# Kernel tuning notes

Measured on AMD Instinct MI355X. Metric: run time of the kernel, lower is better.

## Reference

```python
import jax, jax.numpy as jnp
import numpy as np
import math

H = 8
D_MODEL = 512
D_K = D_MODEL // H          # 64, per-head value dim
D_QK = D_K // 2             # 32, per-head query/key dim
B, S = 2, 4096


def setup_inputs() -> dict:
    key = jax.random.key(0)
    ks = jax.random.split(key, 20)
    std = 0.02
    inp = {
        'query': jax.random.normal(ks[0], (B, S, D_MODEL), jnp.float32),
        'key':   jax.random.normal(ks[1], (B, S, D_MODEL), jnp.float32),
        'value': jax.random.normal(ks[2], (B, S, D_MODEL), jnp.float32),
        # MLP_q: d_model -> 2*d_model -> d_model/2
        'Wq1': jax.random.normal(ks[3], (D_MODEL, 2 * D_MODEL), jnp.float32) * std,
        'bq1': jnp.zeros((2 * D_MODEL,), jnp.float32),
        'Wq2': jax.random.normal(ks[4], (2 * D_MODEL, D_MODEL // 2), jnp.float32) * std,
        'bq2': jnp.zeros((D_MODEL // 2,), jnp.float32),
        # MLP_k: d_model -> 2*d_model -> d_model/2
        'Wk1': jax.random.normal(ks[5], (D_MODEL, 2 * D_MODEL), jnp.float32) * std,
        'bk1': jnp.zeros((2 * D_MODEL,), jnp.float32),
        'Wk2': jax.random.normal(ks[6], (2 * D_MODEL, D_MODEL // 2), jnp.float32) * std,
        'bk2': jnp.zeros((D_MODEL // 2,), jnp.float32),
        # linear_v and output linear: d_model -> d_model
        'Wv': jax.random.normal(ks[7], (D_MODEL, D_MODEL), jnp.float32) * std,
        'bv': jnp.zeros((D_MODEL,), jnp.float32),
        'Wo': jax.random.normal(ks[8], (D_MODEL, D_MODEL), jnp.float32) * std,
        'bo': jnp.zeros((D_MODEL,), jnp.float32),
    }
    return inp


def reference(query, key, value, Wq1, bq1, Wq2, bq2, Wk1, bk1, Wk2, bk2, Wv, bv, Wo, bo):
    nb = query.shape[0]
    # MLP_q / MLP_k: Linear -> exact GELU -> Linear (torch GELU default is erf)
    q = jax.nn.gelu(query @ Wq1 + bq1, approximate=False) @ Wq2 + bq2   # [B,S,D_MODEL/2]
    k = jax.nn.gelu(key   @ Wk1 + bk1, approximate=False) @ Wk2 + bk2   # [B,S,D_MODEL/2]
    v = value @ Wv + bv                                                  # [B,S,D_MODEL]

    q = q.reshape(nb, -1, H, D_QK)   # [B,S,H,d_qk]
    k = k.reshape(nb, -1, H, D_QK)
    v = v.reshape(nb, -1, H, D_K)    # [B,S,H,d_k]

    # scores scaled by sqrt(d_qk) since query.size(-1) == d_k//2 in the original
    scores = jnp.einsum('bqhd,bkhd->bhqk', q, k) / math.sqrt(D_QK)  # [B,H,S,S]
    p = jax.nn.softmax(scores, axis=-1)
    x = jnp.einsum('bhqk,bkhd->bqhd', p, v).reshape(nb, -1, H * D_K)  # [B,S,D_MODEL]
    return x @ Wo + bo
```

## Files before the change

### kernel.cpp

```cpp
#include <hip/hip_runtime.h>
#include <math.h>

typedef __attribute__((ext_vector_type(8))) short short8;
typedef __bf16 bf16x8 __attribute__((ext_vector_type(8)));
typedef __attribute__((ext_vector_type(4))) float f32x4;
typedef __attribute__((ext_vector_type(2))) float f32x2;
typedef __attribute__((ext_vector_type(16))) float f32x16;
typedef __attribute__((ext_vector_type(4))) unsigned uint4v;

__device__ inline short f2bf(float f) {
    unsigned u = __builtin_bit_cast(unsigned, f);
    u += 0x7fff + ((u >> 16) & 1);
    return (short)(u >> 16);
}
__device__ inline float gelu_f(float x) {
    return 0.5f * x * (1.f + erff(x * 0.70710678118654752f));
}

__device__ inline void gload_lds16(const void* g, void* l) {
    __builtin_amdgcn_global_load_lds(
        (const __attribute__((address_space(1))) unsigned int*)g,
        (__attribute__((address_space(3))) unsigned int*)l, 16, 0, 0);
}

__global__ __launch_bounds__(256) void prep_w(
    const float* __restrict__ Wq1, const float* __restrict__ Wk1,
    const float* __restrict__ Wq2, const float* __restrict__ Wk2,
    const float* __restrict__ Wv,  const float* __restrict__ Wo,
    short* __restrict__ Wq1t, short* __restrict__ Wk1t,
    short* __restrict__ Wq2t, short* __restrict__ Wk2t,
    short* __restrict__ Wvt,  short* __restrict__ Wot)
{
    int id = blockIdx.x;
    const float* W; short* Wt; int K, N;
    if (id < 512)       { W = Wq1; Wt = Wq1t; K = 512;  N = 1024; }
    else if (id < 1024) { W = Wk1; Wt = Wk1t; K = 512;  N = 1024; id -= 512; }
    else if (id < 1280) { W = Wq2; Wt = Wq2t; K = 1024; N = 256;  id -= 1024; }
    else if (id < 1536) { W = Wk2; Wt = Wk2t; K = 1024; N = 256;  id -= 1280; }
    else if (id < 1792) { W = Wv;  Wt = Wvt;  K = 512;  N = 512;  id -= 1536; }
    else                { W = Wo;  Wt = Wot;  K = 512;  N = 512;  id -= 1792; }
    int nx = N >> 5;
    int n0 = (id % nx) * 32, k0 = (id / nx) * 32;

    __shared__ float T[32][33];
    int tid = threadIdx.x;
    int r = tid >> 3, c4 = (tid & 7) * 4;
    float4 v4 = *(const float4*)&W[(size_t)(k0 + r) * N + n0 + c4];
    T[r][c4 + 0] = v4.x; T[r][c4 + 1] = v4.y; T[r][c4 + 2] = v4.z; T[r][c4 + 3] = v4.w;
    __syncthreads();
    short4 o;
    o.x = f2bf(T[c4 + 0][r]);
    o.y = f2bf(T[c4 + 1][r]);
    o.z = f2bf(T[c4 + 2][r]);
    o.w = f2bf(T[c4 + 3][r]);
    *(short4*)&Wt[(size_t)(n0 + r) * K + k0 + c4] = o;
}

template <int BM, int BN, int AF32>
__device__ __forceinline__ void gemm_core(
    const void* __restrict__ A, const short* __restrict__ B,
    const float* __restrict__ bias, void* __restrict__ C_,
    float scale, int act, int om, int nbn, int N, int K, int L)
{
    constexpr int MT = BM / 32;
    constexpr int NT = BN / 32;
    const int xcd = L & 7;
    const int per = L >> 3;
    const int bn = (per % nbn) * BN;
    const int bm = ((per / nbn) * 8 + xcd) * BM;

    const int tid = threadIdx.x;
    const int w = tid >> 6;
    const int lane = tid & 63;
    const int l15 = lane & 15, quad = lane >> 4;
    const int wm = (w >> 1) * (BM / 2), wn = (w & 1) * (BN / 2);

    __shared__ __align__(16) short As0[BM * 64], As1[BM * 64];
    __shared__ __align__(16) short Bs0[BN * 64], Bs1[BN * 64];

    const float* Af = (const float*)A;
    const short* Ab = (const short*)A;

    float4 xa[BM / 32], ya[BM / 32];

    auto issue = [&](int k0, short* Asb, short* Bsb) {
#pragma unroll
        for (int i = 0; i < BM / 32; ++i) {
            int ga = tid + i * 256;
            int row = ga >> 3, g = ga & 7;
            if constexpr (AF32) {
                const float* src = &Af[(size_t)(bm + row) * K + k0 + ((g ^ (row & 7)) * 8)];
                xa[i] = *(const float4*)src;
                ya[i] = *(const float4*)(src + 4);
            } else {
                gload_lds16(&Ab[(size_t)(bm + row) * K + k0 + ((g ^ (row & 7)) * 8)],
                            &Asb[(i * 256 + w * 64) * 8]);
            }
        }
#pragma unroll
        for (int i = 0; i < BN / 32; ++i) {
            int gb = tid + i * 256;
            int row = gb >> 3, g = gb & 7;
            gload_lds16(&B[(size_t)(bn + row) * K + k0 + ((g ^ (row & 7)) * 8)],
                        &Bsb[(i * 256 + w * 64) * 8]);
        }
    };
    auto finishA = [&](short* Asb) {
        if constexpr (AF32) {
#pragma unroll
            for (int i = 0; i < BM / 32; ++i) {
                int ga = tid + i * 256;
                int row = ga >> 3, g = ga & 7;
                unsigned u0, u1, u2, u3;
                asm("v_cvt_pk_bf16_f32 %0, %1, %2" : "=v"(u0) : "v"(xa[i].x), "v"(xa[i].y));
                asm("v_cvt_pk_bf16_f32 %0, %1, %2" : "=v"(u1) : "v"(xa[i].z), "v"(xa[i].w));
                asm("v_cvt_pk_bf16_f32 %0, %1, %2" : "=v"(u2) : "v"(ya[i].x), "v"(ya[i].y));
                asm("v_cvt_pk_bf16_f32 %0, %1, %2" : "=v"(u3) : "v"(ya[i].z), "v"(ya[i].w));
                uint4v u; u[0] = u0; u[1] = u1; u[2] = u2; u[3] = u3;
                *(uint4v*)(void*)&Asb[row * 64 + g * 8] = u;
            }
        }
    };

    f32x4 acc[MT][NT];
#pragma unroll
    for (int mt = 0; mt < MT; ++mt)
#pragma unroll
        for (int nt = 0; nt < NT; ++nt) acc[mt][nt] = (f32x4){0.f, 0.f, 0.f, 0.f};

    auto compute = [&](const short* Asc, const short* Bsc) {
#pragma unroll
        for (int ks = 0; ks < 2; ++ks) {
            bf16x8 af[MT], bfr[NT];
#pragma unroll
            for (int t2 = 0; t2 < MT; ++t2) {
                int row = wm + t2 * 16 + l15;
                af[t2] = __builtin_bit_cast(bf16x8,
                    *(const short8*)(const void*)&Asc[row * 64 + (((ks * 4 + quad) ^ (row & 7)) * 8)]);
            }
#pragma unroll
            for (int t2 = 0; t2 < NT; ++t2) {
                int row = wn + t2 * 16 + l15;
                bfr[t2] = __builtin_bit_cast(bf16x8,
                    *(const short8*)(const void*)&Bsc[row * 64 + (((ks * 4 + quad) ^ (row & 7)) * 8)]);
            }
#pragma unroll
            for (int mt = 0; mt < MT; ++mt)
#pragma unroll
                for (int nt = 0; nt < NT; ++nt)
                    acc[mt][nt] = __builtin_amdgcn_mfma_f32_16x16x32_bf16(af[mt], bfr[nt], acc[mt][nt], 0, 0, 0);
        }
    };

    const int ntile = K >> 6;

    issue(0, As0, Bs0);
    finishA(As0);
    __syncthreads();

    for (int t = 0; t < ntile; t += 2) {
        issue((t + 1) << 6, As1, Bs1);
        compute(As0, Bs0);
        finishA(As1);
        __syncthreads();
        if (t + 2 < ntile) issue((t + 2) << 6, As0, Bs0);
        compute(As1, Bs1);
        if (t + 2 < ntile) finishA(As0);
        __syncthreads();
    }

    float bvv[NT];
#pragma unroll
    for (int nt = 0; nt < NT; ++nt) bvv[nt] = bias[bn + wn + nt * 16 + l15];
#pragma unroll
    for (int mt = 0; mt < MT; ++mt)
#pragma unroll
        for (int r = 0; r < 4; ++r) {
            int row = bm + wm + mt * 16 + quad * 4 + r;
#pragma unroll
            for (int nt = 0; nt < NT; ++nt) {
                float v = acc[mt][nt][r] + bvv[nt];
                if (act) v = gelu_f(v);
                v *= scale;
                int col = bn + wn + nt * 16 + l15;
                if (om == 1) {
                    ((float*)C_)[(size_t)row * N + col] = v;
                } else if (om == 2) {
                    int b_ = row >> 12, key = row & 4095;
                    int kt = key >> 6, nt_ = (key >> 5) & 1, l31_ = key & 31;
                    int h_ = col >> 5, kcol = col & 31;
                    int ks_ = kcol >> 4, hi_ = (kcol >> 3) & 1, j_ = kcol & 7;
                    size_t idx = ((((size_t)(b_ * 8 + h_) * 64 + kt) * 4 +
                                   (nt_ * 2 + ks_)) * 64 + (hi_ * 32 + l31_)) * 8 + j_;
                    ((short*)C_)[idx] = f2bf(v);
                } else if (om == 3) {
                    int b_ = row >> 12, key = row & 4095;
                    int kt = key >> 6, keyr = key & 63;
                    int ks_ = keyr >> 4, hi_ = (keyr >> 3) & 1, j_ = keyr & 7;
                    int h_ = col >> 6, dk = col & 63;
                    int dt_ = dk >> 5, l31_ = dk & 31;
                    size_t idx = ((((size_t)(b_ * 8 + h_) * 64 + kt) * 8 +
                                   (dt_ * 4 + ks_)) * 64 + (hi_ * 32 + l31_)) * 8 + j_;
                    ((short*)C_)[idx] = f2bf(v);
                } else {
                    ((short*)C_)[(size_t)row * N + col] = f2bf(v);
                }
            }
        }
}

__global__ __launch_bounds__(256) void mega1(
    const float* __restrict__ q, const float* __restrict__ k,
    const float* __restrict__ v,
    const short* __restrict__ Wq1t, const short* __restrict__ Wk1t,
    const short* __restrict__ Wvt,
    const float* __restrict__ bq1, const float* __restrict__ bk1,
    const float* __restrict__ bv,
    short* __restrict__ H1q, short* __restrict__ H1k, short* __restrict__ vfr)
{
    const int z = blockIdx.z;
    if (z == 2 && blockIdx.x >= 1024) return;
    const float* A   = z == 2 ? v    : (z == 1 ? k    : q);
    const short* B   = z == 2 ? Wvt  : (z == 1 ? Wk1t : Wq1t);
    const float* bia = z == 2 ? bv   : (z == 1 ? bk1  : bq1);
    void*        C   = z == 2 ? (void*)vfr : (z == 1 ? (void*)H1k : (void*)H1q);
    const int act = z == 2 ? 0 : 1;
    const int om  = z == 2 ? 3 : 0;
    const int nbn = z == 2 ? 8 : 16;
    const int N   = z == 2 ? 512 : 1024;
    gemm_core<64, 64, 1>(A, B, bia, C, 1.f, act, om, nbn, N, 512, blockIdx.x);
}

__global__ __launch_bounds__(256) void gemm2k(
    const short* __restrict__ H1q, const short* __restrict__ H1k,
    const short* __restrict__ Wq2t, const short* __restrict__ Wk2t,
    const float* __restrict__ bq2, const float* __restrict__ bk2,
    short* __restrict__ qbb, short* __restrict__ kfr, float qscale)
{
    const int z = blockIdx.z;
    const short* A   = z ? H1k : H1q;
    const short* B   = z ? Wk2t : Wq2t;
    const float* bia = z ? bk2 : bq2;
    void*        C   = z ? (void*)kfr : (void*)qbb;
    const float  sc  = z ? 1.f : qscale;
    const int    om  = z ? 2 : 0;
    gemm_core<64, 64, 0>(A, B, bia, C, sc, 0, om, 4, 256, 1024, blockIdx.x);
}

__global__ __launch_bounds__(256) void gemmok(
    const short* __restrict__ xbb, const short* __restrict__ Wot,
    const float* __restrict__ bo, float* __restrict__ out)
{
    gemm_core<64, 64, 0>(xbb, Wot, bo, out, 1.f, 0, 1, 8, 512, 512, blockIdx.x);
}

__global__ __launch_bounds__(256, 4) void flash_ks(
    const short* __restrict__ qb, const short* __restrict__ kfr,
    const short* __restrict__ vfr, short* __restrict__ xbb)
{
    const int L = blockIdx.x;
    const int xcd = L & 7;
    const int idx = L >> 3;
    const int bh = xcd * 2 + (idx & 1);
    const int qt = idx >> 1;
    const int b = bh >> 3, h = bh & 7;
    const int w = threadIdx.x >> 6;
    const int qg = w >> 1;
    const int kh = w & 1;
    const int lane = threadIdx.x & 63;
    const int l31 = lane & 31;
    const int half = lane >> 5;

    __shared__ __align__(16) char smem[17408];

    const short* qrow = qb + (size_t)(b * 4096 + qt * 64 + qg * 32 + l31) * 256 + h * 32 + half * 8;
    bf16x8 qf0 = __builtin_bit_cast(bf16x8, *(const short8*)(const void*)qrow);
    bf16x8 qf1 = __builtin_bit_cast(bf16x8, *(const short8*)(const void*)(qrow + 16));

    f32x16 O0{}, O1{};
    f32x2 lp = (f32x2){0.f, 0.f};

    const short* kbase = kfr + ((size_t)bh * 64) * 4 * 512 + lane * 8;
    const short* vbase = vfr + ((size_t)bh * 64) * 8 * 512 + lane * 8;

#pragma unroll 1
    for (int t = 0; t < 32; ++t) {
        const int kt = kh * 32 + t;
        bf16x8 kc[4], vc[8];
        const short* kp = kbase + (size_t)kt * 4 * 512;
        const short* vp = vbase + (size_t)kt * 8 * 512;
#pragma unroll
        for (int c = 0; c < 4; ++c)
            kc[c] = __builtin_bit_cast(bf16x8, *(const short8*)(const void*)(kp + c * 512));
#pragma unroll
        for (int c = 0; c < 8; ++c)
            vc[c] = __builtin_bit_cast(bf16x8, *(const short8*)(const void*)(vp + c * 512));

        f32x16 zero{};
        f32x16 s0 = __builtin_amdgcn_mfma_f32_32x32x16_bf16(kc[0], qf0, zero, 0, 0, 0);
        s0 = __builtin_amdgcn_mfma_f32_32x32x16_bf16(kc[1], qf1, s0, 0, 0, 0);
        f32x16 s1 = __builtin_amdgcn_mfma_f32_32x32x16_bf16(kc[2], qf0, zero, 0, 0, 0);
        s1 = __builtin_amdgcn_mfma_f32_32x32x16_bf16(kc[3], qf1, s1, 0, 0, 0);

        bf16x8 pf[4];
#pragma unroll
        for (int nt = 0; nt < 2; ++nt) {
            const f32x16& s = nt ? s1 : s0;
            float p0  = __builtin_amdgcn_exp2f(s[0]);
            float p1  = __builtin_amdgcn_exp2f(s[1]);
            float p2  = __builtin_amdgcn_exp2f(s[2]);
            float p3  = __builtin_amdgcn_exp2f(s[3]);
            float p4  = __builtin_amdgcn_exp2f(s[4]);
            float p5  = __builtin_amdgcn_exp2f(s[5]);
            float p6  = __builtin_amdgcn_exp2f(s[6]);
            float p7  = __builtin_amdgcn_exp2f(s[7]);
            float p8  = __builtin_amdgcn_exp2f(s[8]);
            float p9  = __builtin_amdgcn_exp2f(s[9]);
            float p10 = __builtin_amdgcn_exp2f(s[10]);
            float p11 = __builtin_amdgcn_exp2f(s[11]);
            float p12 = __builtin_amdgcn_exp2f(s[12]);
            float p13 = __builtin_amdgcn_exp2f(s[13]);
            float p14 = __builtin_amdgcn_exp2f(s[14]);
            float p15 = __builtin_amdgcn_exp2f(s[15]);

            lp += (f32x2){p0,  p1};
            lp += (f32x2){p2,  p3};
            lp += (f32x2){p4,  p5};
            lp += (f32x2){p6,  p7};
            lp += (f32x2){p8,  p9};
            lp += (f32x2){p10, p11};
            lp += (f32x2){p12, p13};
            lp += (f32x2){p14, p15};

            unsigned D0, D1, D2, D3, D4, D5, D6, D7;
            asm("v_cvt_pk_bf16_f32 %0, %1, %2" : "=v"(D0) : "v"(p0),  "v"(p1));
            asm("v_cvt_pk_bf16_f32 %0, %1, %2" : "=v"(D1) : "v"(p2),  "v"(p3));
            asm("v_cvt_pk_bf16_f32 %0, %1, %2" : "=v"(D2) : "v"(p4),  "v"(p5));
            asm("v_cvt_pk_bf16_f32 %0, %1, %2" : "=v"(D3) : "v"(p6),  "v"(p7));
            asm("v_cvt_pk_bf16_f32 %0, %1, %2" : "=v"(D4) : "v"(p8),  "v"(p9));
            asm("v_cvt_pk_bf16_f32 %0, %1, %2" : "=v"(D5) : "v"(p10), "v"(p11));
            asm("v_cvt_pk_bf16_f32 %0, %1, %2" : "=v"(D6) : "v"(p12), "v"(p13));
            asm("v_cvt_pk_bf16_f32 %0, %1, %2" : "=v"(D7) : "v"(p14), "v"(p15));
            asm("v_permlane32_swap_b32 %0, %1" : "+v"(D0), "+v"(D2));
            asm("v_permlane32_swap_b32 %0, %1" : "+v"(D1), "+v"(D3));
            asm("v_permlane32_swap_b32 %0, %1" : "+v"(D4), "+v"(D6));
            asm("v_permlane32_swap_b32 %0, %1" : "+v"(D5), "+v"(D7));
            uint4v u0; u0[0] = D0; u0[1] = D1; u0[2] = D2; u0[3] = D3;
            uint4v u1; u1[0] = D4; u1[1] = D5; u1[2] = D6; u1[3] = D7;
            pf[2 * nt + 0] = __builtin_bit_cast(bf16x8, u0);
            pf[2 * nt + 1] = __builtin_bit_cast(bf16x8, u1);
        }

#pragma unroll
        for (int ks = 0; ks < 4; ++ks) {
            O0 = __builtin_amdgcn_mfma_f32_32x32x16_bf16(pf[ks], vc[ks], O0, 0, 0, 0);
            O1 = __builtin_amdgcn_mfma_f32_32x32x16_bf16(pf[ks], vc[4 + ks], O1, 0, 0, 0);
        }
    }

    float lsum = lp[0] + lp[1];
    float lother = lsum;
    asm("v_permlane32_swap_b32 %0, %1" : "+v"(lsum), "+v"(lother));
    lsum += lother;

    float* redO = (float*)smem;
    float* redl = (float*)(smem + 16896);
    if (half == 0)
        redl[(qg * 2 + kh) * 32 + l31] = lsum;
    if (kh == 1) {
        float* Bo = redO + qg * 32 * 66;
#pragma unroll
        for (int r = 0; r < 16; ++r) {
            int q = (r & 3) + 8 * (r >> 2) + 4 * half;
            Bo[q * 66 + l31] = O0[r];
            Bo[q * 66 + 32 + l31] = O1[r];
        }
    }
    __syncthreads();
    if (kh == 0) {
        const float* Bo = redO + qg * 32 * 66;
#pragma unroll
        for (int r = 0; r < 16; ++r) {
            int q = (r & 3) + 8 * (r >> 2) + 4 * half;
            float o0 = O0[r] + Bo[q * 66 + l31];
            float o1 = O1[r] + Bo[q * 66 + 32 + l31];
            float inv = 1.f / (redl[(qg * 2 + 0) * 32 + q] + redl[(qg * 2 + 1) * 32 + q]);
            size_t row = (size_t)(b * 4096 + qt * 64 + qg * 32 + q);
            short* d = xbb + row * 512 + h * 64 + l31;
            d[0] = f2bf(o0 * inv);
            d[32] = f2bf(o1 * inv);
        }
    }
}

extern "C" void kernel_launch(void* const* d_in, const int* in_sizes, int n_in,
                              void* d_out, int out_size, void* d_ws, size_t ws_size,
                              hipStream_t stream)
{
    const float* query = (const float*)d_in[0];
    const float* key   = (const float*)d_in[1];
    const float* value = (const float*)d_in[2];
    const float* Wq1   = (const float*)d_in[3];
    const float* bq1   = (const float*)d_in[4];
    const float* Wq2   = (const float*)d_in[5];
    const float* bq2   = (const float*)d_in[6];
    const float* Wk1   = (const float*)d_in[7];
    const float* bk1   = (const float*)d_in[8];
    const float* Wk2   = (const float*)d_in[9];
    const float* bk2   = (const float*)d_in[10];
    const float* Wv    = (const float*)d_in[11];
    const float* bv    = (const float*)d_in[12];
    const float* Wo    = (const float*)d_in[13];
    const float* bo    = (const float*)d_in[14];
    float* out = (float*)d_out;

    char* ws = (char*)d_ws;
    short* H1q   = (short*)(ws + 0);
    short* H1k   = (short*)(ws + 16777216);
    short* xbb   = (short*)(ws + 0);
    short* qbb   = (short*)(ws + 33554432);
    short* kfr   = (short*)(ws + 50331648);
    short* vfr   = (short*)(ws + 54525952);
    short* Wq1t  = (short*)(ws + 62914560);
    short* Wk1t  = (short*)(ws + 63963136);
    short* Wq2t  = (short*)(ws + 65011712);
    short* Wk2t  = (short*)(ws + 65536000);
    short* Wvt   = (short*)(ws + 66060288);
    short* Wot   = (short*)(ws + 66584576);

    dim3 blk(256);
    const float qscale = 0.17677669529663687f * 1.4426950408889634f;

    prep_w<<<dim3(2048), blk, 0, stream>>>(
        Wq1, Wk1, Wq2, Wk2, Wv, Wo, Wq1t, Wk1t, Wq2t, Wk2t, Wvt, Wot);

    mega1<<<dim3(2048, 1, 3), blk, 0, stream>>>(
        query, key, value, Wq1t, Wk1t, Wvt, bq1, bk1, bv, H1q, H1k, vfr);

    gemm2k<<<dim3(512, 1, 2), blk, 0, stream>>>(
        H1q, H1k, Wq2t, Wk2t, bq2, bk2, qbb, kfr, qscale);

    flash_ks<<<dim3(1024), blk, 0, stream>>>(qbb, kfr, vfr, xbb);

    gemmok<<<dim3(1024), blk, 0, stream>>>(xbb, Wot, bo, out);
}
```

Baseline: 257.6 us.

## Deepen GEMM double-buffer prefetch with explicit vmcnt waits and raw barriers

Restructures the GEMM main loop so the next tile's global-to-LDS loads are issued a full tile ahead and kept in flight across barriers. Full __syncthreads is replaced by raw s_barrier plus partial s_waitcnt vmcnt counts, so only the older loads must finish before compute. This aims to hide global memory latency behind MFMA work. It relies on hand-counted outstanding loads per issue (6 or 4), which breaks correctness if the issue pattern changes, and it adds extra barriers per iteration.

```diff
diff --git a/kernel.cpp b/kernel.cpp
--- a/kernel.cpp
+++ b/kernel.cpp
@@ -22,6 +22,14 @@
         (const __attribute__((address_space(1))) unsigned int*)g,
         (__attribute__((address_space(3))) unsigned int*)l, 16, 0, 0);
 }
+
+#define GBARRIER do { asm volatile("" ::: "memory"); \
+                      __builtin_amdgcn_s_barrier();  \
+                      asm volatile("" ::: "memory"); } while (0)
+#define VMCNT6 asm volatile("s_waitcnt vmcnt(6)" ::: "memory")
+#define VMCNT4 asm volatile("s_waitcnt vmcnt(4)" ::: "memory")
+#define VMCNT0 asm volatile("s_waitcnt vmcnt(0)" ::: "memory")
+#define LGKM0  asm volatile("s_waitcnt lgkmcnt(0)" ::: "memory")
 
 __global__ __launch_bounds__(256) void prep_w(
     const float* __restrict__ Wq1, const float* __restrict__ Wk1,
@@ -156,17 +164,31 @@
 
     issue(0, As0, Bs0);
     finishA(As0);
-    __syncthreads();
-
+    issue(1 << 6, As1, Bs1);
+    if constexpr (AF32) { VMCNT6; } else { VMCNT4; }
+    LGKM0;
+    GBARRIER;
+
+#pragma unroll 1
     for (int t = 0; t < ntile; t += 2) {
-        issue((t + 1) << 6, As1, Bs1);
+        const bool h2 = (t + 2 < ntile);
+        const bool h3 = (t + 3 < ntile);
         compute(As0, Bs0);
         finishA(As1);
-        __syncthreads();
-        if (t + 2 < ntile) issue((t + 2) << 6, As0, Bs0);
+        GBARRIER;
+        if (h2) issue((t + 2) << 6, As0, Bs0);
+        if constexpr (AF32) { if (h2) { VMCNT6; } else { VMCNT0; } }
+        else                { if (h2) { VMCNT4; } else { VMCNT0; } }
+        LGKM0;
+        GBARRIER;
         compute(As1, Bs1);
-        if (t + 2 < ntile) finishA(As0);
-        __syncthreads();
+        if (h2) finishA(As0);
+        GBARRIER;
+        if (h3) issue((t + 3) << 6, As1, Bs1);
+        if constexpr (AF32) { if (h3) { VMCNT6; } else { VMCNT0; } }
+        else                { if (h3) { VMCNT4; } else { VMCNT0; } }
+        LGKM0;
+        GBARRIER;
     }
 
     float bvv[NT];
```

Measured after the change: 268.3 us. 4.1% more time.
